# Kernel optimization log

Hardware: AMD Instinct MI355X
Metric: run time of the kernel (lower is better)

The kernel has to match this reference:

```python
import jax, jax.numpy as jnp
import numpy as np


def _haar_filters():
    # pywt 'haar': dec_lo = [s, s], dec_hi = [-s, s], s = 1/sqrt(2)
    s = np.float32(1.0 / np.sqrt(2.0))
    lo = np.array([s, s], dtype=np.float32)
    hi = np.array([-s, s], dtype=np.float32)
    # torch conv2d is cross-correlation; filter_2d = outer(row, col)
    # order matches module output concat: LL, LH, HL, HH
    f = np.stack([
        np.outer(lo, lo),  # LL
        np.outer(lo, hi),  # LH
        np.outer(hi, lo),  # HL
        np.outer(hi, hi),  # HH
    ]).astype(np.float32)  # (4, 2, 2)
    return jnp.asarray(f)


def setup_inputs() -> dict:
    key = jax.random.key(0)
    x = jax.random.normal(key, (8, 32, 512, 512), dtype=jnp.float32)
    return {"x": x, "filters": _haar_filters()}


def reference(x, filters):
    """Haar DWT2D: (B,C,H,W) -> (B,4C,H//2+1,W//2+1).

    Matches torch: pad to even dims (zeros), reflect-pad by 1,
    2x2 cross-correlation with stride 2 per subband, channel-concat
    [LL | LH | HL | HH].
    """
    b, c, h, w = x.shape
    pad_h = (2 - h % 2) % 2
    pad_w = (2 - w % 2) % 2
    if pad_h or pad_w:  # static shapes -> jit-safe Python branch
        x = jnp.pad(x, ((0, 0), (0, 0), (0, pad_h), (0, pad_w)))
    xp = jnp.pad(x, ((0, 0), (0, 0), (1, 1), (1, 1)), mode="reflect")
    # Stride-2 2x2 windows: tap (di,dj) of window (i,j) is xp[2i+di, 2j+dj].
    # xp has H+2 rows -> H//2 + 1 window rows (same for cols).
    x00 = xp[:, :, 0::2, 0::2]
    x01 = xp[:, :, 0::2, 1::2]
    x10 = xp[:, :, 1::2, 0::2]
    x11 = xp[:, :, 1::2, 1::2]
    win = jnp.stack([x00, x01, x10, x11], axis=-1)  # (B,C,h2,w2,4)
    f = filters.reshape(4, 4)                        # (subband, tap)
    out = jnp.einsum("bchwt,kt->bkchw", win, f)      # (B,4,C,h2,w2)
    b_, k_, c_, h2, w2 = out.shape
    return out.reshape(b_, k_ * c_, h2, w2)


if __name__ == "__main__":
    inp = setup_inputs()
    y = reference(**inp)
    print(y.shape, y.dtype)
```

## Files before the change

kernel.cpp:

```cpp
#include <hip/hip_runtime.h>


constexpr int H_IN  = 512;
constexpr int W_IN  = 512;
constexpr int H_OUT = 257;
constexpr int W_OUT = 257;
constexpr long long PLANE_OUT = (long long)H_OUT * W_OUT;
constexpr long long PLANE_IN  = (long long)H_IN * W_IN;

typedef float f2v __attribute__((ext_vector_type(2), aligned(4)));

__global__ __launch_bounds__(256)
void dwt2d_haar_reg(const float* __restrict__ x,
                    const float* __restrict__ filt,
                    float* __restrict__ out) {
    const int t  = threadIdx.x;
    const int j  = t & 127;
    const int i  = blockIdx.x * 2 + (t >> 7);
    const int bc = blockIdx.y;
    if (i >= H_OUT) return;

    int r0 = 2 * i - 1; if (r0 < 0)     r0 = 1;
    int r1 = 2 * i;     if (r1 >= H_IN) r1 = H_IN - 2;

    const float* xp = x + (long long)bc * PLANE_IN;
    const float4 v0 = *reinterpret_cast<const float4*>(xp + r0 * W_IN + 4 * j);
    const float4 v1 = *reinterpret_cast<const float4*>(xp + r1 * W_IN + 4 * j);

    float p0 = __shfl_up(v0.w, 1);
    float p1 = __shfl_up(v1.w, 1);
    if ((t & 63) == 0) {
        if (j == 0) { p0 = v0.y; p1 = v1.y; }
        else        { p0 = xp[r0 * W_IN + 4 * j - 1];
                      p1 = xp[r1 * W_IN + 4 * j - 1]; }
    }

    float F[16];
#pragma unroll
    for (int k = 0; k < 16; ++k) F[k] = filt[k];

    const int bb = bc >> 5, cc = bc & 31;
    const long long obase = (long long)(bb * 128 + cc) * PLANE_OUT
                          + (long long)i * W_OUT;

#pragma unroll
    for (int k = 0; k < 4; ++k) {
        float o0 = F[4*k+0]*p0   + F[4*k+1]*v0.x + F[4*k+2]*p1   + F[4*k+3]*v1.x;
        float o1 = F[4*k+0]*v0.y + F[4*k+1]*v0.z + F[4*k+2]*v1.y + F[4*k+3]*v1.z;
        f2v o; o.x = o0; o.y = o1;
        __builtin_nontemporal_store(
            o, reinterpret_cast<f2v*>(&out[obase + (long long)(k * 32) * PLANE_OUT + 2 * j]));
    }
    if (j == 127) {
#pragma unroll
        for (int k = 0; k < 4; ++k) {
            float o = F[4*k+0]*v0.w + F[4*k+1]*v0.z + F[4*k+2]*v1.w + F[4*k+3]*v1.z;
            __builtin_nontemporal_store(
                o, &out[obase + (long long)(k * 32) * PLANE_OUT + 256]);
        }
    }
}

extern "C" void kernel_launch(void* const* d_in, const int* in_sizes, int n_in,
                              void* d_out, int out_size, void* d_ws, size_t ws_size,
                              hipStream_t stream) {
    const float* x    = (const float*)d_in[0];
    const float* filt = (const float*)d_in[1];
    float*       out  = (float*)d_out;

    dim3 grid((H_OUT + 1) / 2, 256);
    dwt2d_haar_reg<<<grid, 256, 0, stream>>>(x, filt, out);
}
```

Baseline: 100.3 us.

## Process two output rows per thread with offset unaligned loads replacing shuffles

Each block now covers four output rows instead of two, so each thread handles two rows and issues four 16-byte loads up front for more memory-level parallelism. The left-neighbour value now comes from loading the float4 one element earlier (unaligned) rather than through a cross-lane shuffle plus fallback scalar loads, and the last column gets a separate scalar tail load. 64-bit index math is replaced with 32-bit ints. Risks: the unaligned vector loads may split across cache lines, and the grid is halved, which lowers occupancy.

Result: faster. 94.95 us (-5.3%).

```diff
diff --git a/kernel.cpp b/kernel.cpp
--- a/kernel.cpp
+++ b/kernel.cpp
@@ -5,60 +5,81 @@
 constexpr int W_IN  = 512;
 constexpr int H_OUT = 257;
 constexpr int W_OUT = 257;
-constexpr long long PLANE_OUT = (long long)H_OUT * W_OUT;
-constexpr long long PLANE_IN  = (long long)H_IN * W_IN;
+constexpr int PLANE_OUT = H_OUT * W_OUT;
+constexpr int PLANE_IN  = H_IN * W_IN;
 
+typedef float f4v __attribute__((ext_vector_type(4), aligned(4)));
 typedef float f2v __attribute__((ext_vector_type(2), aligned(4)));
 
 __global__ __launch_bounds__(256)
-void dwt2d_haar_reg(const float* __restrict__ x,
-                    const float* __restrict__ filt,
-                    float* __restrict__ out) {
+void dwt2d_haar_r5(const float* __restrict__ x,
+                   const float* __restrict__ filt,
+                   float* __restrict__ out) {
     const int t  = threadIdx.x;
     const int j  = t & 127;
-    const int i  = blockIdx.x * 2 + (t >> 7);
+    const int s  = t >> 7;
     const int bc = blockIdx.y;
-    if (i >= H_OUT) return;
+    const int i0 = blockIdx.x * 4;
 
-    int r0 = 2 * i - 1; if (r0 < 0)     r0 = 1;
-    int r1 = 2 * i;     if (r1 >= H_IN) r1 = H_IN - 2;
+    const int  iA = i0 + s;
+    const int  iB = iA + 2;
+    const bool vA = (iA < H_OUT);
+    const bool vB = (iB < H_OUT);
+    const int  iAc = vA ? iA : (H_OUT - 1);
+    const int  iBc = vB ? iB : (H_OUT - 1);
 
-    const float* xp = x + (long long)bc * PLANE_IN;
-    const float4 v0 = *reinterpret_cast<const float4*>(xp + r0 * W_IN + 4 * j);
-    const float4 v1 = *reinterpret_cast<const float4*>(xp + r1 * W_IN + 4 * j);
+    const float* xp = x + bc * PLANE_IN;
+    const int  cb   = (j == 0) ? 0 : (4 * j - 1);
+    const bool tail = (j == 127);
 
-    float p0 = __shfl_up(v0.w, 1);
-    float p1 = __shfl_up(v1.w, 1);
-    if ((t & 63) == 0) {
-        if (j == 0) { p0 = v0.y; p1 = v1.y; }
-        else        { p0 = xp[r0 * W_IN + 4 * j - 1];
-                      p1 = xp[r1 * W_IN + 4 * j - 1]; }
+    int rA0 = 2 * iAc - 1; if (rA0 < 0)     rA0 = 1;
+    int rA1 = 2 * iAc;     if (rA1 >= H_IN) rA1 = H_IN - 2;
+    int rB0 = 2 * iBc - 1;
+    int rB1 = 2 * iBc;     if (rB1 >= H_IN) rB1 = H_IN - 2;
+
+    float tA0 = 0.f, tA1 = 0.f, tB0 = 0.f, tB1 = 0.f;
+    if (tail) {
+        tA0 = xp[rA0 * W_IN + 511]; tA1 = xp[rA1 * W_IN + 511];
+        tB0 = xp[rB0 * W_IN + 511]; tB1 = xp[rB1 * W_IN + 511];
     }
+
+    f4v vA0 = *reinterpret_cast<const f4v*>(xp + rA0 * W_IN + cb);
+    f4v vA1 = *reinterpret_cast<const f4v*>(xp + rA1 * W_IN + cb);
+    f4v vB0 = *reinterpret_cast<const f4v*>(xp + rB0 * W_IN + cb);
+    f4v vB1 = *reinterpret_cast<const f4v*>(xp + rB1 * W_IN + cb);
 
     float F[16];
 #pragma unroll
     for (int k = 0; k < 16; ++k) F[k] = filt[k];
 
     const int bb = bc >> 5, cc = bc & 31;
-    const long long obase = (long long)(bb * 128 + cc) * PLANE_OUT
-                          + (long long)i * W_OUT;
+    const int pbase = (bb * 128 + cc) * PLANE_OUT;
 
-#pragma unroll
-    for (int k = 0; k < 4; ++k) {
-        float o0 = F[4*k+0]*p0   + F[4*k+1]*v0.x + F[4*k+2]*p1   + F[4*k+3]*v1.x;
-        float o1 = F[4*k+0]*v0.y + F[4*k+1]*v0.z + F[4*k+2]*v1.y + F[4*k+3]*v1.z;
-        f2v o; o.x = o0; o.y = o1;
-        __builtin_nontemporal_store(
-            o, reinterpret_cast<f2v*>(&out[obase + (long long)(k * 32) * PLANE_OUT + 2 * j]));
-    }
-    if (j == 127) {
+    auto emit = [&](int i, const f4v& v0, const f4v& v1,
+                    float t0, float t1, bool valid) {
+        if (!valid) return;
+        float a0 = j ? v0.x : v0.y,  b0 = j ? v0.y : v0.x;
+        float a1 = j ? v1.x : v1.y,  b1 = j ? v1.y : v1.x;
+        float c0 = j ? v0.z : v0.y,  d0 = j ? v0.w : v0.z;
+        float c1 = j ? v1.z : v1.y,  d1 = j ? v1.w : v1.z;
+        const int rbase = pbase + i * W_OUT;
 #pragma unroll
         for (int k = 0; k < 4; ++k) {
-            float o = F[4*k+0]*v0.w + F[4*k+1]*v0.z + F[4*k+2]*v1.w + F[4*k+3]*v1.z;
+            float oe = F[4*k]*a0 + F[4*k+1]*b0 + F[4*k+2]*a1 + F[4*k+3]*b1;
+            float oo = F[4*k]*c0 + F[4*k+1]*d0 + F[4*k+2]*c1 + F[4*k+3]*d1;
+            f2v o; o.x = oe; o.y = oo;
             __builtin_nontemporal_store(
-                o, &out[obase + (long long)(k * 32) * PLANE_OUT + 256]);
+                o, reinterpret_cast<f2v*>(&out[rbase + k * 32 * PLANE_OUT + 2 * j]));
+            if (tail) {
+                float ot = F[4*k]*t0 + F[4*k+1]*v0.w + F[4*k+2]*t1 + F[4*k+3]*v1.w;
+                __builtin_nontemporal_store(
+                    ot, &out[rbase + k * 32 * PLANE_OUT + 256]);
+            }
         }
-    }
+    };
+
+    emit(iA, vA0, vA1, tA0, tA1, vA);
+    emit(iB, vB0, vB1, tB0, tB1, vB);
 }
 
 extern "C" void kernel_launch(void* const* d_in, const int* in_sizes, int n_in,
@@ -68,6 +89,6 @@
     const float* filt = (const float*)d_in[1];
     float*       out  = (float*)d_out;
 
-    dim3 grid((H_OUT + 1) / 2, 256);
-    dwt2d_haar_reg<<<grid, 256, 0, stream>>>(x, filt, out);
+    dim3 grid((H_OUT + 3) / 4, 256);
+    dwt2d_haar_r5<<<grid, 256, 0, stream>>>(x, filt, out);
 }
```
